# Kernel optimization log

Measured on AMD Instinct MI355X. Metric: run time of the kernel, lower is better.

The kernel has to match this reference:

```python
import jax, jax.numpy as jnp
import numpy as np

B_SZ, NX, IN_DIM = 32, 16384, 3
DIM, J, MODE, RANK, FC_DIM, OUT_DIM, N_LAYERS = 64, 16, 128, 4, 128, 1, 3


def setup_inputs() -> dict:
    key = jax.random.key(0)
    ks = jax.random.split(key, 20)
    scale = 1.0 / (MODE * MODE)
    s_out = 1.0 / MODE
    x = jax.random.normal(ks[0], (B_SZ, NX, IN_DIM), jnp.float32)
    bases = jax.random.normal(ks[1], (NX, MODE), jnp.float32) / np.sqrt(NX)
    wbases = jax.random.normal(ks[2], (NX, MODE), jnp.float32) / np.sqrt(NX)
    product = bases.T @ wbases  # (MODE_out, MODE_in)
    D_out = np.sqrt(s_out) * jax.random.uniform(ks[3], (J, MODE), jnp.float32)
    D_in = np.sqrt(s_out) * jax.random.uniform(ks[4], (J, MODE), jnp.float32)
    A = s_out * jax.random.uniform(ks[5], (J, RANK, MODE), jnp.float32)
    Bm = s_out * jax.random.uniform(ks[6], (J, RANK, MODE), jnp.float32)
    W_sp = scale * jax.random.normal(ks[7], (N_LAYERS, DIM, DIM, J), jnp.float32)
    W_conv = jax.random.normal(ks[8], (N_LAYERS, DIM, DIM), jnp.float32) / np.sqrt(DIM)
    b_conv = jnp.zeros((N_LAYERS, DIM), jnp.float32)
    W0 = jax.random.normal(ks[9], (IN_DIM, DIM), jnp.float32) / np.sqrt(IN_DIM)
    b0 = jnp.zeros((DIM,), jnp.float32)
    W1 = jax.random.normal(ks[10], (DIM, FC_DIM), jnp.float32) / np.sqrt(DIM)
    b1 = jnp.zeros((FC_DIM,), jnp.float32)
    W2 = jax.random.normal(ks[11], (FC_DIM, OUT_DIM), jnp.float32) / np.sqrt(FC_DIM)
    b2 = jnp.zeros((OUT_DIM,), jnp.float32)
    return {"x": x, "bases": bases, "wbases": wbases, "product": product,
            "D_out": D_out, "D_in": D_in, "A": A, "Bm": Bm,
            "W_sp": W_sp, "W_conv": W_conv, "b_conv": b_conv,
            "W0": W0, "b0": b0, "W1": W1, "b1": b1, "W2": W2, "b2": b2}


def reference(x, bases, wbases, product, D_out, D_in, A, Bm, W_sp, W_conv, b_conv,
              W0, b0, W1, b1, W2, b2):
    # fc0: (b, nx, in_dim) -> (b, nx, dim), then channel-first (b, dim, nx)
    h = jnp.swapaxes(x @ W0 + b0, 1, 2)
    # H construction: diag outer-products + low-rank A^T B update (mask_mode=0 so full add)
    H = D_out[:, :, None] * D_in[:, None, :] * product[None] \
        + jnp.einsum('jrk,jrl->jkl', A, Bm)  # (J, MODE, MODE)
    for i in range(N_LAYERS):
        xh = jnp.einsum('bcx,xk->bck', h, wbases)          # spectral transform
        xh1 = jnp.einsum('jkl,bil->bijk', H, xh)           # H mixing
        y = jnp.einsum('ioj,bijk->bok', W_sp[i], xh1)      # channel/kernel contraction
        x1 = jnp.einsum('bck,xk->bcx', y, bases)           # inverse transform
        x2 = jnp.einsum('oc,bcx->box', W_conv[i], h) + b_conv[i][None, :, None]
        h = x1 + x2
        if i != N_LAYERS - 1:
            h = jax.nn.gelu(h, approximate=False)
    h = jnp.swapaxes(h, 1, 2)  # (b, nx, dim)
    h = jax.nn.gelu(h @ W1 + b1, approximate=False)
    return h @ W2 + b2
```

## Files before the change

### kernel.cpp

```cpp
#include <hip/hip_runtime.h>
#include <hip/hip_bf16.h>
#include <math.h>

#define B_SZ   32
#define NXX    16384
#define IN_DIM 3
#define DIM    64
#define JM     16
#define MODE   128
#define RANKK  4
#define FC_DIM 128
#define N_LAY  3

typedef __attribute__((ext_vector_type(8))) short bf16x8;
typedef __attribute__((ext_vector_type(4))) float f32x4;
typedef unsigned short u16;

__device__ __forceinline__ float gelu_fast(float v) {
    float p = v * (0.7978845608f + 0.0356774081f * v * v);
    float e = __expf(-2.f * p);
    return v * __builtin_amdgcn_rcpf(1.f + e);
}
__device__ __forceinline__ u16 to_bf16(float v) {
    __hip_bfloat16 b = __float2bfloat16(v);
    return *(u16*)&b;
}

__global__ __launch_bounds__(256) void k_zero(float* __restrict__ p, int n) {
    int i = blockIdx.x * 256 + threadIdx.x;
    if (i < n) p[i] = 0.f;
}

__global__ __launch_bounds__(256) void k_build_H(
        const float* __restrict__ Dout, const float* __restrict__ Din,
        const float* __restrict__ product, const float* __restrict__ A,
        const float* __restrict__ Bm, u16* __restrict__ Hbf) {
    int idx = blockIdx.x * 256 + threadIdx.x;
    int j = idx >> 14;
    int k = (idx >> 7) & 127;
    int l = idx & 127;
    float v = Dout[j * MODE + k] * Din[j * MODE + l] * product[k * MODE + l];
#pragma unroll
    for (int r = 0; r < RANKK; ++r)
        v += A[(j * RANKK + r) * MODE + k] * Bm[(j * RANKK + r) * MODE + l];
    Hbf[idx] = to_bf16(v);
}

__global__ __launch_bounds__(256) void k_setup_wst(
        const float* __restrict__ Wsp, u16* __restrict__ WsT) {
    int idx = blockIdx.x * 256 + threadIdx.x;
    int i = idx & 63, o = (idx >> 6) & 63, j = (idx >> 12) & 15, lay = idx >> 16;
    WsT[idx] = to_bf16(Wsp[(((size_t)lay * 64 + i) * 64 + o) * 16 + j]);
}

__global__ __launch_bounds__(256) void k_setup_bases(
        const float* __restrict__ bases, u16* __restrict__ bh) {
    int idx = blockIdx.x * 256 + threadIdx.x;
    int x = idx >> 7, k = idx & 127;
    size_t off = (size_t)(k >> 3) * 131072 + (size_t)x * 8 + (k & 7);
    bh[off] = to_bf16(bases[idx]);
}

__global__ __launch_bounds__(256) void k_setup_wbT(
        const float* __restrict__ wb, u16* __restrict__ Th) {
    __shared__ float tile[32][33];
    int bx = blockIdx.x, bl = blockIdx.y;
    int t = threadIdx.x;
    int i = t >> 5, jj = t & 31;
#pragma unroll
    for (int r = 0; r < 4; ++r)
        tile[i + r * 8][jj] = wb[(size_t)(bx * 32 + i + r * 8) * MODE + bl * 32 + jj];
    __syncthreads();
#pragma unroll
    for (int r = 0; r < 4; ++r) {
        int l = bl * 32 + i + r * 8;
        int x = bx * 32 + jj;
        Th[(size_t)l * NXX + x] = to_bf16(tile[jj][i + r * 8]);
    }
}

__global__ __launch_bounds__(256) void k_setup_w1t(
        const float* __restrict__ W1, u16* __restrict__ wh) {
    int i = blockIdx.x * 256 + threadIdx.x;
    int f = i >> 6, c = i & 63;
    wh[i] = to_bf16(W1[c * FC_DIM + f]);
}

__global__ __launch_bounds__(256) void k_fc0(
        const float* __restrict__ x, const float* __restrict__ W0,
        const float* __restrict__ b0, u16* __restrict__ hh) {
    __shared__ float w0s[IN_DIM * DIM + DIM];
    int t = threadIdx.x;
    if (t < IN_DIM * DIM) w0s[t] = W0[t];
    if (t < DIM) w0s[IN_DIM * DIM + t] = b0[t];
    __syncthreads();
    int b = blockIdx.y;
    int xi = blockIdx.x * 32 + (t >> 3);
    int c8 = (t & 7) * 8;
    const float* xp = x + ((size_t)b * NXX + xi) * IN_DIM;
    float x0 = xp[0], x1 = xp[1], x2 = xp[2];
    u16 rh[8];
#pragma unroll
    for (int i = 0; i < 8; ++i) {
        int c = c8 + i;
        float v = x0 * w0s[c] + x1 * w0s[DIM + c] + x2 * w0s[2 * DIM + c]
                + w0s[3 * DIM + c];
        rh[i] = to_bf16(v);
    }
    size_t o = ((size_t)(b << 14) + xi) * 64 + c8;
    *(ushort4*)(hh + o)     = make_ushort4(rh[0], rh[1], rh[2], rh[3]);
    *(ushort4*)(hh + o + 4) = make_ushort4(rh[4], rh[5], rh[6], rh[7]);
}

#define SPAD 72
__global__ __launch_bounds__(256) void k_spectral_mfma(
        const u16* __restrict__ Hh,
        const u16* __restrict__ Wh,
        float* __restrict__ xh) {
    __shared__ u16 Ash[64 * SPAD];
    int t = threadIdx.x;
    int wave = t >> 6, lane = t & 63, quad = lane >> 4, l16 = lane & 15;
    int lin = blockIdx.y * 32 + blockIdx.x;
    int swz = (lin & 7) * 128 + (lin >> 3);
    int b = swz & 31;
    int x0 = (swz >> 5) * 512;
    int cq = (t & 15) * 4;
    int xq = (t >> 4) * 4;
    int colw = (xq + ((t & 7) << 3)) & 63;
    const u16* srch = Hh + ((size_t)(b << 14) + x0 + xq) * 64 + cq;
    int l0 = wave * 32;
    const u16* w0h = Wh + (size_t)(l0 + l16) * NXX + x0;
    const u16* w1h = Wh + (size_t)(l0 + 16 + l16) * NXX + x0;
    ushort4 r0, r1, r2, r3;
    {
        const u16* s = srch;
        r0 = *(const ushort4*)(s);
        r1 = *(const ushort4*)(s + 64);
        r2 = *(const ushort4*)(s + 128);
        r3 = *(const ushort4*)(s + 192);
    }
    f32x4 acc[4][2] = {};
    for (int kt = 0; kt < 512; kt += 64) {
        __syncthreads();
        *(ushort4*)&Ash[(cq + 0) * SPAD + colw] = make_ushort4(r0.x, r1.x, r2.x, r3.x);
        *(ushort4*)&Ash[(cq + 1) * SPAD + colw] = make_ushort4(r0.y, r1.y, r2.y, r3.y);
        *(ushort4*)&Ash[(cq + 2) * SPAD + colw] = make_ushort4(r0.z, r1.z, r2.z, r3.z);
        *(ushort4*)&Ash[(cq + 3) * SPAD + colw] = make_ushort4(r0.w, r1.w, r2.w, r3.w);
        if (kt + 64 < 512) {
            const u16* s = srch + (size_t)(kt + 64) * 64;
            r0 = *(const ushort4*)(s);
            r1 = *(const ushort4*)(s + 64);
            r2 = *(const ushort4*)(s + 128);
            r3 = *(const ushort4*)(s + 192);
        }
        __builtin_amdgcn_sched_barrier(0);
        __syncthreads();
#pragma unroll
        for (int k0 = 0; k0 < 64; k0 += 32) {
            bf16x8 afh[4];
#pragma unroll
            for (int ct = 0; ct < 4; ++ct) {
                int rr = ct * 16 + l16;
                int ro = rr * SPAD + (((k0 + quad * 8) + (((rr >> 2) & 7) << 3)) & 63);
                afh[ct] = *(const bf16x8*)&Ash[ro];
            }
            int go = kt + k0 + quad * 8;
            bf16x8 b0h = *(const bf16x8*)(w0h + go);
            bf16x8 b1h = *(const bf16x8*)(w1h + go);
#pragma unroll
            for (int ct = 0; ct < 4; ++ct) {
                acc[ct][0] = __builtin_amdgcn_mfma_f32_16x16x32_bf16(afh[ct], b0h, acc[ct][0], 0, 0, 0);
                acc[ct][1] = __builtin_amdgcn_mfma_f32_16x16x32_bf16(afh[ct], b1h, acc[ct][1], 0, 0, 0);
            }
        }
    }
    float* xb = xh + (size_t)(b << 6) * 128;
#pragma unroll
    for (int ct = 0; ct < 4; ++ct)
#pragma unroll
        for (int lt = 0; lt < 2; ++lt)
#pragma unroll
            for (int r = 0; r < 4; ++r)
                atomicAdd(xb + (size_t)(ct * 16 + quad * 4 + r) * 128 + l0 + lt * 16 + l16,
                          acc[ct][lt][r]);
}

#define XPAD 136
#define TPAD 72
__global__ __launch_bounds__(256) void k_hmix_mfma(
        const float* __restrict__ xh, const u16* __restrict__ Hbf,
        const u16* __restrict__ WsT, float* __restrict__ y, int lay) {
    __shared__ u16 xsb[64 * XPAD];
    __shared__ u16 Ts[128 * TPAD];
    int t = threadIdx.x;
    int wave = t >> 6, lane = t & 63, quad = lane >> 4, l16 = lane & 15;
    int b = blockIdx.x, j = blockIdx.y;
    const float* xb = xh + (size_t)b * DIM * MODE;
    for (int idx = t; idx < DIM * MODE; idx += 256)
        xsb[(idx >> 7) * XPAD + (idx & 127)] = to_bf16(xb[idx]);
    __syncthreads();
    int k_base = wave * 32;
    {
        f32x4 acc[2][4] = {};
        const u16* Hj = Hbf + (size_t)j * MODE * MODE;
#pragma unroll
        for (int l0 = 0; l0 < 128; l0 += 32) {
            bf16x8 af[2], bf[4];
#pragma unroll
            for (int mt = 0; mt < 2; ++mt)
                af[mt] = *(const bf16x8*)(Hj + (size_t)(k_base + mt * 16 + l16) * 128 + l0 + quad * 8);
#pragma unroll
            for (int nt = 0; nt < 4; ++nt)
                bf[nt] = *(const bf16x8*)&xsb[(nt * 16 + l16) * XPAD + l0 + quad * 8];
#pragma unroll
            for (int mt = 0; mt < 2; ++mt)
#pragma unroll
                for (int nt = 0; nt < 4; ++nt)
                    acc[mt][nt] = __builtin_amdgcn_mfma_f32_16x16x32_bf16(af[mt], bf[nt], acc[mt][nt], 0, 0, 0);
        }
#pragma unroll
        for (int mt = 0; mt < 2; ++mt)
#pragma unroll
            for (int nt = 0; nt < 4; ++nt)
#pragma unroll
                for (int r = 0; r < 4; ++r)
                    Ts[(k_base + mt * 16 + quad * 4 + r) * TPAD + nt * 16 + l16] =
                        to_bf16(acc[mt][nt][r]);
    }
    __syncthreads();
    {
        f32x4 acc[4][2] = {};
        const u16* Wj = WsT + ((size_t)lay * JM + j) * DIM * DIM;
#pragma unroll
        for (int i0 = 0; i0 < 64; i0 += 32) {
            bf16x8 af[4], bf[2];
#pragma unroll
            for (int mt = 0; mt < 4; ++mt)
                af[mt] = *(const bf16x8*)(Wj + (size_t)(mt * 16 + l16) * 64 + i0 + quad * 8);
#pragma unroll
            for (int nt = 0; nt < 2; ++nt)
                bf[nt] = *(const bf16x8*)&Ts[(k_base + nt * 16 + l16) * TPAD + i0 + quad * 8];
#pragma unroll
            for (int mt = 0; mt < 4; ++mt)
#pragma unroll
                for (int nt = 0; nt < 2; ++nt)
                    acc[mt][nt] = __builtin_amdgcn_mfma_f32_16x16x32_bf16(af[mt], bf[nt], acc[mt][nt], 0, 0, 0);
        }
        float* yb = y + (size_t)b * DIM * MODE;
#pragma unroll
        for (int mt = 0; mt < 4; ++mt)
#pragma unroll
            for (int nt = 0; nt < 2; ++nt)
#pragma unroll
                for (int r = 0; r < 4; ++r)
                    atomicAdd(yb + (size_t)(mt * 16 + quad * 4 + r) * 128 + k_base + nt * 16 + l16,
                              acc[mt][nt][r]);
    }
}

__global__ __launch_bounds__(256) void k_build_A(
        const float* __restrict__ y, const float* __restrict__ Wconv,
        u16* __restrict__ Ah, int lay) {
    int b = blockIdx.x;
    for (int idx = threadIdx.x; idx < 12288; idx += 256) {
        int i = idx & 7, l16 = (idx >> 3) & 15, quad = (idx >> 7) & 3,
            ot = (idx >> 9) & 3, ks = idx >> 11;
        int o = ot * 16 + l16;
        int k = ks * 32 + quad * 8 + i;
        float v = (k < 128) ? y[((size_t)b * DIM + o) * MODE + k]
                            : Wconv[(size_t)lay * DIM * DIM + o * DIM + (k - 128)];
        Ah[(size_t)b * 12288 + idx] = to_bf16(v);
    }
}

template <bool DO_MLP>
__global__ __launch_bounds__(256, 4) void k_inv_conv_mfma(
        const u16* __restrict__ Afh,
        const u16* __restrict__ Bfh,
        u16* __restrict__ Hh,
        const float* __restrict__ bconv, int lay,
        const u16* __restrict__ W1h,
        const float* __restrict__ b1, const float* __restrict__ W2,
        const float* __restrict__ b2, float* __restrict__ out) {
    __shared__ u16 sh[12288];
    int t = threadIdx.x;
    int wave = t >> 6, lane = t & 63, quad = lane >> 4, l16 = lane & 15;
    int bid = blockIdx.x;
    int swz = (bid & 7) * 512 + (bid >> 3);
    int b = swz & 31;
    int x0 = (swz >> 5) * 128;
    int xw = wave * 32;

    const u16* afb = Afh + (size_t)b * 12288;
    bf16x8 areg[6];
#pragma unroll
    for (int i = 0; i < 6; ++i)
        areg[i] = *(const bf16x8*)(afb + (size_t)(i * 256 + t) * 8);
    bf16x8 bg[4][2], hf[2][2];
#pragma unroll
    for (int ks = 0; ks < 4; ++ks)
#pragma unroll
        for (int x2 = 0; x2 < 2; ++x2) {
            int xl = xw + x2 * 16 + l16;
            bg[ks][x2] = *(const bf16x8*)(Bfh + (size_t)((ks * 4 + quad) * 16384 + x0 + xl) * 8);
        }
#pragma unroll
    for (int ks = 0; ks < 2; ++ks)
#pragma unroll
        for (int x2 = 0; x2 < 2; ++x2) {
            int xl = xw + x2 * 16 + l16;
            hf[ks][x2] = *(const bf16x8*)(Hh + ((size_t)(b << 14) + x0 + xl) * 64
                                          + ks * 32 + quad * 8);
        }
    __builtin_amdgcn_sched_barrier(0);
#pragma unroll
    for (int i = 0; i < 6; ++i)
        *(bf16x8*)&sh[(i * 256 + t) * 8] = areg[i];
    __syncthreads();

    f32x4 acc[4][2] = {};
#pragma unroll
    for (int ks = 0; ks < 6; ++ks) {
        bf16x8 afh[4];
#pragma unroll
        for (int ot = 0; ot < 4; ++ot)
            afh[ot] = *(const bf16x8*)&sh[(((ks * 4 + ot) * 4 + quad) * 16 + l16) * 8];
#pragma unroll
        for (int ot = 0; ot < 4; ++ot)
#pragma unroll
            for (int x2 = 0; x2 < 2; ++x2)
                acc[ot][x2] = __builtin_amdgcn_mfma_f32_16x16x32_bf16(
                    afh[ot], ks < 4 ? bg[ks][x2] : hf[ks - 4][x2],
                    acc[ot][x2], 0, 0, 0);
    }
    __syncthreads();

#pragma unroll
    for (int ot = 0; ot < 4; ++ot) {
        float4 bc = *(const float4*)(bconv + lay * DIM + ot * 16 + quad * 4);
#pragma unroll
        for (int x2 = 0; x2 < 2; ++x2) {
            int xl = xw + x2 * 16 + l16;
            float vr[4] = {acc[ot][x2][0] + bc.x, acc[ot][x2][1] + bc.y,
                           acc[ot][x2][2] + bc.z, acc[ot][x2][3] + bc.w};
            if (!DO_MLP) {
#pragma unroll
                for (int r = 0; r < 4; ++r) vr[r] = gelu_fast(vr[r]);
            }
            ushort4 uh;
            uh.x = to_bf16(vr[0]); uh.y = to_bf16(vr[1]);
            uh.z = to_bf16(vr[2]); uh.w = to_bf16(vr[3]);
            int col = ot * 16 + quad * 4;
            *(ushort4*)&sh[xl * 64 + (col ^ ((xl & 7) << 3))] = uh;
        }
    }

    if (!DO_MLP) {
        __syncthreads();
#pragma unroll
        for (int it = 0; it < 4; ++it) {
            int idx = it * 256 + t;
            int row = idx >> 3, c8 = (idx & 7) * 8;
            size_t dst = ((size_t)(b << 14) + x0 + row) * 64 + c8;
            *(bf16x8*)(Hh + dst) =
                *(const bf16x8*)&sh[row * 64 + (c8 ^ ((row & 7) << 3))];
        }
        return;
    }

#pragma unroll
    for (int x2 = 0; x2 < 2; ++x2) {
        int xl = xw + x2 * 16 + l16;
        bf16x8 ah[2];
#pragma unroll
        for (int ks = 0; ks < 2; ++ks) {
            int ko = ks * 32 + quad * 8;
            ah[ks] = *(const bf16x8*)&sh[xl * 64 + (ko ^ ((xl & 7) << 3))];
        }
        float vo[4] = {0.f, 0.f, 0.f, 0.f};
#pragma unroll
        for (int ft = 0; ft < 8; ++ft) {
            f32x4 a2 = {};
#pragma unroll
            for (int ks = 0; ks < 2; ++ks) {
                size_t o = (size_t)(ft * 16 + l16) * 64 + ks * 32 + quad * 8;
                bf16x8 bh = *(const bf16x8*)(W1h + o);
                a2 = __builtin_amdgcn_mfma_f32_16x16x32_bf16(ah[ks], bh, a2, 0, 0, 0);
            }
            float bb = b1[ft * 16 + l16];
            float w2 = W2[ft * 16 + l16];
#pragma unroll
            for (int r = 0; r < 4; ++r)
                vo[r] += gelu_fast(a2[r] + bb) * w2;
        }
#pragma unroll
        for (int r = 0; r < 4; ++r) {
            float v = vo[r];
            v += __shfl_xor(v, 1);
            v += __shfl_xor(v, 2);
            v += __shfl_xor(v, 4);
            v += __shfl_xor(v, 8);
            vo[r] = v;
        }
        if (l16 == 0) {
            float bb2 = b2[0];
            float4 o4 = make_float4(vo[0] + bb2, vo[1] + bb2,
                                    vo[2] + bb2, vo[3] + bb2);
            *(float4*)(out + (size_t)b * NXX + x0 + xw + x2 * 16 + quad * 4) = o4;
        }
    }
}

extern "C" void kernel_launch(void* const* d_in, const int* in_sizes, int n_in,
                              void* d_out, int out_size, void* d_ws, size_t ws_size,
                              hipStream_t stream) {
    const float* x      = (const float*)d_in[0];
    const float* bases  = (const float*)d_in[1];
    const float* wbases = (const float*)d_in[2];
    const float* product= (const float*)d_in[3];
    const float* Dout   = (const float*)d_in[4];
    const float* Din    = (const float*)d_in[5];
    const float* A      = (const float*)d_in[6];
    const float* Bm     = (const float*)d_in[7];
    const float* Wsp    = (const float*)d_in[8];
    const float* Wconv  = (const float*)d_in[9];
    const float* bconv  = (const float*)d_in[10];
    const float* W0     = (const float*)d_in[11];
    const float* b0     = (const float*)d_in[12];
    const float* W1     = (const float*)d_in[13];
    const float* b1     = (const float*)d_in[14];
    const float* W2     = (const float*)d_in[15];
    const float* b2     = (const float*)d_in[16];
    float* out = (float*)d_out;

    const size_t need = 79314944;
    if (ws_size < need) {
        k_zero<<<dim3((out_size + 255) / 256), dim3(256), 0, stream>>>(out, out_size);
        return;
    }

    char* W = (char*)d_ws;
    size_t off = 0;
    auto alloc = [&](size_t bytes) { void* p = W + off; off += bytes; return p; };
    u16*   Hbf      = (u16*)alloc(524288);
    u16*   WsT      = (u16*)alloc(393216);
    u16*   bases_hi = (u16*)alloc(4194304);
    u16*   wbT_hi   = (u16*)alloc(4194304);
    u16*   Abuf_hi  = (u16*)alloc(786432);
    float* ybuf     = (float*)alloc(1048576);
    float* xh       = (float*)alloc(1048576);
    u16*   h_hi     = (u16*)alloc(67108864);
    u16*   w1t_hi   = (u16*)alloc(16384);

    k_build_H<<<dim3(1024), dim3(256), 0, stream>>>(Dout, Din, product, A, Bm, Hbf);
    k_setup_wst<<<dim3(768), dim3(256), 0, stream>>>(Wsp, WsT);
    k_setup_bases<<<dim3(8192), dim3(256), 0, stream>>>(bases, bases_hi);
    k_setup_wbT<<<dim3(512, 4), dim3(256), 0, stream>>>(wbases, wbT_hi);
    k_setup_w1t<<<dim3(32), dim3(256), 0, stream>>>(W1, w1t_hi);
    k_fc0<<<dim3(512, B_SZ), dim3(256), 0, stream>>>(x, W0, b0, h_hi);

    for (int lay = 0; lay < N_LAY; ++lay) {
        int last = (lay == N_LAY - 1);
        k_zero<<<dim3(2048), dim3(256), 0, stream>>>(ybuf, 524288);
        k_spectral_mfma<<<dim3(B_SZ, 32), dim3(256), 0, stream>>>(
            h_hi, wbT_hi, xh);
        k_hmix_mfma<<<dim3(B_SZ, JM), dim3(256), 0, stream>>>(
            xh, Hbf, WsT, ybuf, lay);
        k_build_A<<<dim3(B_SZ), dim3(256), 0, stream>>>(ybuf, Wconv, Abuf_hi, lay);
        dim3 g(4096), blk(256);
        if (last)
            k_inv_conv_mfma<true><<<g, blk, 0, stream>>>(
                Abuf_hi, bases_hi, h_hi, bconv, lay,
                w1t_hi, b1, W2, b2, out);
        else
            k_inv_conv_mfma<false><<<g, blk, 0, stream>>>(
                Abuf_hi, bases_hi, h_hi, bconv, lay,
                w1t_hi, b1, W2, b2, out);
    }
}
```

Before: 460.9 us.

## Load A fragments directly to registers and drop shared-memory staging in inverse conv

Each lane now loads its A-operand MFMA fragments straight from global memory into registers (24 bf16x8 per lane), so the block-wide shared-memory staging and its barriers go away. The non-MLP path writes GELU outputs to global memory directly from the accumulators instead of transposing through shared memory, and the MLP path uses a per-wave shared slice that needs no __syncthreads. Launch bounds fall from 4 to 2 blocks per CU to make room for the extra registers. The trade is lower occupancy, redundant global A loads across waves, and narrower 8-byte scattered stores for H.

```diff
diff --git a/kernel.cpp b/kernel.cpp
--- a/kernel.cpp
+++ b/kernel.cpp
@@ -274,7 +274,7 @@
 }
 
 template <bool DO_MLP>
-__global__ __launch_bounds__(256, 4) void k_inv_conv_mfma(
+__global__ __launch_bounds__(256, 2) void k_inv_conv_mfma(
         const u16* __restrict__ Afh,
         const u16* __restrict__ Bfh,
         u16* __restrict__ Hh,
@@ -282,7 +282,7 @@
         const u16* __restrict__ W1h,
         const float* __restrict__ b1, const float* __restrict__ W2,
         const float* __restrict__ b2, float* __restrict__ out) {
-    __shared__ u16 sh[12288];
+    __shared__ u16 osh[DO_MLP ? 4 * 2048 : 8];
     int t = threadIdx.x;
     int wave = t >> 6, lane = t & 63, quad = lane >> 4, l16 = lane & 15;
     int bid = blockIdx.x;
@@ -292,10 +292,12 @@
     int xw = wave * 32;
 
     const u16* afb = Afh + (size_t)b * 12288;
-    bf16x8 areg[6];
-#pragma unroll
-    for (int i = 0; i < 6; ++i)
-        areg[i] = *(const bf16x8*)(afb + (size_t)(i * 256 + t) * 8);
+    bf16x8 af[6][4];
+#pragma unroll
+    for (int ks = 0; ks < 6; ++ks)
+#pragma unroll
+        for (int ot = 0; ot < 4; ++ot)
+            af[ks][ot] = *(const bf16x8*)(afb + (size_t)(((ks * 4 + ot) * 4 + quad) * 16 + l16) * 8);
     bf16x8 bg[4][2], hf[2][2];
 #pragma unroll
     for (int ks = 0; ks < 4; ++ks)
@@ -313,69 +315,61 @@
                                           + ks * 32 + quad * 8);
         }
     __builtin_amdgcn_sched_barrier(0);
-#pragma unroll
-    for (int i = 0; i < 6; ++i)
-        *(bf16x8*)&sh[(i * 256 + t) * 8] = areg[i];
-    __syncthreads();
 
     f32x4 acc[4][2] = {};
 #pragma unroll
-    for (int ks = 0; ks < 6; ++ks) {
-        bf16x8 afh[4];
-#pragma unroll
-        for (int ot = 0; ot < 4; ++ot)
-            afh[ot] = *(const bf16x8*)&sh[(((ks * 4 + ot) * 4 + quad) * 16 + l16) * 8];
+    for (int ks = 0; ks < 6; ++ks)
 #pragma unroll
         for (int ot = 0; ot < 4; ++ot)
 #pragma unroll
             for (int x2 = 0; x2 < 2; ++x2)
                 acc[ot][x2] = __builtin_amdgcn_mfma_f32_16x16x32_bf16(
-                    afh[ot], ks < 4 ? bg[ks][x2] : hf[ks - 4][x2],
+                    af[ks][ot], ks < 4 ? bg[ks][x2] : hf[ks - 4][x2],
                     acc[ot][x2], 0, 0, 0);
-    }
-    __syncthreads();
-
+
+    if (!DO_MLP) {
+#pragma unroll
+        for (int ot = 0; ot < 4; ++ot) {
+            float4 bc = *(const float4*)(bconv + lay * DIM + ot * 16 + quad * 4);
+#pragma unroll
+            for (int x2 = 0; x2 < 2; ++x2) {
+                int xl = xw + x2 * 16 + l16;
+                ushort4 uh;
+                uh.x = to_bf16(gelu_fast(acc[ot][x2][0] + bc.x));
+                uh.y = to_bf16(gelu_fast(acc[ot][x2][1] + bc.y));
+                uh.z = to_bf16(gelu_fast(acc[ot][x2][2] + bc.z));
+                uh.w = to_bf16(gelu_fast(acc[ot][x2][3] + bc.w));
+                *(ushort4*)(Hh + ((size_t)(b << 14) + x0 + xl) * 64
+                            + ot * 16 + quad * 4) = uh;
+            }
+        }
+        return;
+    }
+
+    u16* oshw = &osh[wave * 2048];
 #pragma unroll
     for (int ot = 0; ot < 4; ++ot) {
         float4 bc = *(const float4*)(bconv + lay * DIM + ot * 16 + quad * 4);
 #pragma unroll
         for (int x2 = 0; x2 < 2; ++x2) {
-            int xl = xw + x2 * 16 + l16;
-            float vr[4] = {acc[ot][x2][0] + bc.x, acc[ot][x2][1] + bc.y,
-                           acc[ot][x2][2] + bc.z, acc[ot][x2][3] + bc.w};
-            if (!DO_MLP) {
-#pragma unroll
-                for (int r = 0; r < 4; ++r) vr[r] = gelu_fast(vr[r]);
-            }
+            int rl = x2 * 16 + l16;
             ushort4 uh;
-            uh.x = to_bf16(vr[0]); uh.y = to_bf16(vr[1]);
-            uh.z = to_bf16(vr[2]); uh.w = to_bf16(vr[3]);
+            uh.x = to_bf16(acc[ot][x2][0] + bc.x);
+            uh.y = to_bf16(acc[ot][x2][1] + bc.y);
+            uh.z = to_bf16(acc[ot][x2][2] + bc.z);
+            uh.w = to_bf16(acc[ot][x2][3] + bc.w);
             int col = ot * 16 + quad * 4;
-            *(ushort4*)&sh[xl * 64 + (col ^ ((xl & 7) << 3))] = uh;
-        }
-    }
-
-    if (!DO_MLP) {
-        __syncthreads();
-#pragma unroll
-        for (int it = 0; it < 4; ++it) {
-            int idx = it * 256 + t;
-            int row = idx >> 3, c8 = (idx & 7) * 8;
-            size_t dst = ((size_t)(b << 14) + x0 + row) * 64 + c8;
-            *(bf16x8*)(Hh + dst) =
-                *(const bf16x8*)&sh[row * 64 + (c8 ^ ((row & 7) << 3))];
-        }
-        return;
-    }
-
+            *(ushort4*)&oshw[rl * 64 + (col ^ ((rl & 7) << 3))] = uh;
+        }
+    }
 #pragma unroll
     for (int x2 = 0; x2 < 2; ++x2) {
-        int xl = xw + x2 * 16 + l16;
+        int rl = x2 * 16 + l16;
         bf16x8 ah[2];
 #pragma unroll
         for (int ks = 0; ks < 2; ++ks) {
             int ko = ks * 32 + quad * 8;
-            ah[ks] = *(const bf16x8*)&sh[xl * 64 + (ko ^ ((xl & 7) << 3))];
+            ah[ks] = *(const bf16x8*)&oshw[rl * 64 + (ko ^ ((rl & 7) << 3))];
         }
         float vo[4] = {0.f, 0.f, 0.f, 0.f};
 #pragma unroll
```

Result: slower. 506.5 us (+9.9%).
